# Kernel optimization log

Hardware: AMD Instinct MI355X
Metric: run time of the kernel (lower is better)

## Reference

```python
import jax, jax.numpy as jnp
import numpy as np

B, V, E = 1024, 50257, 128

def setup_inputs() -> dict:
    key = jax.random.key(0)
    k1, k2, k3 = jax.random.split(key, 3)
    # one-hot focus-word vectors [B, V]
    idx = jax.random.randint(k1, (B,), 0, V)
    xs = jax.nn.one_hot(idx, V, dtype=jnp.float32)
    EMBEDM = jax.random.normal(k2, (V, E), dtype=jnp.float32)
    metric = jax.random.normal(k3, (E, E), dtype=jnp.float32)
    return {"xs": xs, "EMBEDM": EMBEDM, "metric": metric}

def reference(xs, EMBEDM, metric):
    # xsembeds = xs @ EMBEDM  -> [B, E] (dense matmul that is mathematically a gather)
    xsembeds = jnp.matmul(xs, EMBEDM)
    # dots(vs, ws, metric) = (vs @ metric) @ ws.T -> [B, V]
    scores = jnp.matmul(jnp.matmul(xsembeds, metric), EMBEDM.T)
    return jax.nn.log_softmax(scores, axis=1)
```

## Files before the change

### kernel.cpp

```cpp
#include <hip/hip_runtime.h>
#include <math.h>

#define BB 1024
#define VV 50257
#define EE 128
#define RR 256
#define CC 1024
#define CH 64
#define NCH (CC / CH)
#define NCB ((VV + CC - 1) / CC)
#define CVTB 2048

typedef __bf16 bf16x8 __attribute__((ext_vector_type(8)));
typedef float f32x4 __attribute__((ext_vector_type(4)));
typedef f32x4 __attribute__((aligned(4))) f32x4u;

typedef __attribute__((address_space(3))) void as3_void;
typedef const __attribute__((address_space(1))) void as1_void;

static __device__ __forceinline__ unsigned short f2bf(float f) {
  unsigned int u = __float_as_uint(f);
  u += 0x7fffu + ((u >> 16) & 1u);
  return (unsigned short)(u >> 16);
}

__global__ __launch_bounds__(256) void k_prep(const float* __restrict__ xs,
                                              const float* __restrict__ em,
                                              const float* __restrict__ metric,
                                              unsigned short* __restrict__ ebf,
                                              unsigned short* __restrict__ ybf) {
  const int t = threadIdx.x;
  if (blockIdx.x < BB) {
    const int b = blockIdx.x;
    __shared__ int found;
    __shared__ int sidx;
    __shared__ float sval;
    __shared__ float x[EE];
    const float* row = xs + (size_t)b * VV;
    if (t == 0) {
      found = 0; sidx = 0; sval = 0.f;
      const float tail = row[VV - 1];
      if (tail != 0.f) { sidx = VV - 1; sval = tail; found = 1; }
    }
    __syncthreads();
    if (!found) {
      for (int base = 0; base < 12564; base += 1024) {
#pragma unroll
        for (int j = 0; j < 4; j++) {
          const int i = base + j * 256 + t;
          if (i < 12564) {
            f32x4u v = *(const f32x4u*)(row + i * 4);
            if (v[0] != 0.f || v[1] != 0.f || v[2] != 0.f || v[3] != 0.f) {
#pragma unroll
              for (int c = 0; c < 4; c++)
                if (v[c] != 0.f) { sidx = i * 4 + c; sval = v[c]; }
              found = 1;
            }
          }
        }
        __syncthreads();
        if (found) break;
      }
    }
    if (t < EE) x[t] = em[(size_t)sidx * EE + t] * sval;
    __syncthreads();
    if (t < EE) {
      float acc = 0.f;
#pragma unroll
      for (int k = 0; k < EE; k++) acc = fmaf(x[k], metric[k * EE + t], acc);
      ybf[b * EE + t] = f2bf(acc);
    }
  } else {
    const int total4 = VV * EE / 4;
    const int stride = CVTB * 256;
    for (int i = (blockIdx.x - BB) * 256 + t; i < total4; i += stride) {
      float4 v = ((const float4*)em)[i];
      ushort4 o;
      o.x = f2bf(v.x); o.y = f2bf(v.y); o.z = f2bf(v.z); o.w = f2bf(v.w);
      ((ushort4*)ebf)[i] = o;
    }
  }
}


static __device__ __forceinline__ void stageE(const unsigned short* __restrict__ ebf,
                                              char* ldsbuf, int colbase, int w, int lane) {
#pragma unroll
  for (int i = 0; i < 2; i++) {
    const int G = (i * 8 + w) * 64 + lane;
    const int c2 = G >> 4;
    const int gc = G & 15;
    int col = colbase + c2;
    col = col < VV ? col : VV - 1;
    const char* src = (const char*)(ebf + (size_t)col * EE) + ((gc ^ (c2 & 7)) * 16);
    __builtin_amdgcn_global_load_lds((as1_void*)src,
                                     (as3_void*)(ldsbuf + (i * 8 + w) * 1024), 16, 0, 0);
  }
}

template <bool PASS_B, bool TAIL>
static __device__ __forceinline__ void gemm_body(const unsigned short* __restrict__ ybf,
                                                 const unsigned short* __restrict__ ebf,
                                                 char* __restrict__ ldsE,
                                                 float* __restrict__ pm, float* __restrict__ ps,
                                                 const float* __restrict__ lse,
                                                 float* __restrict__ out) {
  const int cbx = blockIdx.x;
  const int rowbase = blockIdx.y * RR;
  const int w = threadIdx.x >> 6;
  const int l = threadIdx.x & 63;
  const int g = l >> 4;
  const int li = l & 15;
  const int rg = w >> 1;
  const int cg = w & 1;
  const int cb = cbx * CC;

  bf16x8 y[4][4];
#pragma unroll
  for (int rf = 0; rf < 4; rf++) {
    const bf16x8* yv = (const bf16x8*)(ybf + (size_t)(rowbase + rg * 64 + rf * 16 + li) * EE);
#pragma unroll
    for (int kk = 0; kk < 4; kk++) y[rf][kk] = yv[kk * 4 + g];
  }

  float Lr[4];
  float m[4], s[4];
  if (PASS_B) {
#pragma unroll
    for (int rf = 0; rf < 4; rf++) Lr[rf] = lse[rowbase + rg * 64 + rf * 16 + li];
  } else {
#pragma unroll
    for (int rf = 0; rf < 4; rf++) { m[rf] = -INFINITY; s[rf] = 0.f; }
  }

  stageE(ebf, ldsE, cb, w, l);
  __syncthreads();

#pragma unroll 2
  for (int k = 0; k < NCH; k++) {
    if (k + 1 < NCH) stageE(ebf, ldsE + ((k + 1) & 1) * 16384, cb + (k + 1) * CH, w, l);

    const char* cur = ldsE + (k & 1) * 16384;
    bf16x8 afr[2][4];
#pragma unroll
    for (int cf = 0; cf < 2; cf++) {
      const int c2 = cg * 32 + cf * 16 + li;
      const char* ebase = cur + c2 * 256;
#pragma unroll
      for (int kk = 0; kk < 4; kk++)
        afr[cf][kk] = *(const bf16x8*)(ebase + (((kk * 4 + g) ^ (li & 7)) * 16));
    }

    f32x4 acc[4][2];
#pragma unroll
    for (int rf = 0; rf < 4; rf++)
#pragma unroll
      for (int cf = 0; cf < 2; cf++) acc[rf][cf] = (f32x4){0.f, 0.f, 0.f, 0.f};
#pragma unroll
    for (int rf = 0; rf < 4; rf++)
#pragma unroll
      for (int cf = 0; cf < 2; cf++)
#pragma unroll
        for (int kk = 0; kk < 4; kk++)
          acc[rf][cf] = __builtin_amdgcn_mfma_f32_16x16x32_bf16(afr[cf][kk], y[rf][kk],
                                                                acc[rf][cf], 0, 0, 0);

    const int colk = cb + k * CH + cg * 32 + g * 4;

    if (!PASS_B) {
#pragma unroll
      for (int rf = 0; rf < 4; rf++) {
        float cm = -INFINITY;
#pragma unroll
        for (int cf = 0; cf < 2; cf++)
#pragma unroll
          for (int r = 0; r < 4; r++)
            if (!TAIL || colk + cf * 16 + r < VV) cm = fmaxf(cm, acc[rf][cf][r]);
        const float mn = fmaxf(m[rf], cm);
        if (!TAIL || mn > -INFINITY) {
          float as = s[rf] * __expf(m[rf] - mn);
#pragma unroll
          for (int cf = 0; cf < 2; cf++)
#pragma unroll
            for (int r = 0; r < 4; r++)
              if (!TAIL || colk + cf * 16 + r < VV) as += __expf(acc[rf][cf][r] - mn);
          s[rf] = as; m[rf] = mn;
        }
      }
    } else {
#pragma unroll
      for (int rf = 0; rf < 4; rf++) {
        float* orow = out + (size_t)(rowbase + rg * 64 + rf * 16 + li) * VV;
#pragma unroll
        for (int cf = 0; cf < 2; cf++) {
          const int c = colk + cf * 16;
          if (!TAIL || c + 3 < VV) {
            f32x4 v;
#pragma unroll
            for (int r = 0; r < 4; r++) v[r] = acc[rf][cf][r] - Lr[rf];
            *(f32x4u*)(orow + c) = v;
          } else {
#pragma unroll
            for (int r = 0; r < 4; r++)
              if (c + r < VV) orow[c + r] = acc[rf][cf][r] - Lr[rf];
          }
        }
      }
    }

    __syncthreads();
  }

  if (!PASS_B) {
#pragma unroll
    for (int off = 16; off <= 32; off <<= 1) {
#pragma unroll
      for (int rf = 0; rf < 4; rf++) {
        const float mo = __shfl_xor(m[rf], off);
        const float so = __shfl_xor(s[rf], off);
        const float mn = fmaxf(m[rf], mo);
        float sn;
        if (mn == -INFINITY) sn = 0.f;
        else sn = s[rf] * __expf(m[rf] - mn) + so * __expf(mo - mn);
        m[rf] = mn; s[rf] = sn;
      }
    }
    float* scm = (float*)ldsE;
    float* scs = scm + 512;
    __syncthreads();
    if (l < 16) {
#pragma unroll
      for (int rf = 0; rf < 4; rf++) {
        const int slot = ((rg * 2 + cg) * 4 + rf) * 16 + li;
        scm[slot] = m[rf]; scs[slot] = s[rf];
      }
    }
    __syncthreads();
    const int t = threadIdx.x;
    if (t < 256) {
      const int trg = t >> 6, trf = (t >> 4) & 3, tli = t & 15;
      const int s0 = ((trg * 2 + 0) * 4 + trf) * 16 + tli;
      const int s1 = ((trg * 2 + 1) * 4 + trf) * 16 + tli;
      const float m0 = scm[s0], m1 = scm[s1];
      const float mn = fmaxf(m0, m1);
      float sn;
      if (mn == -INFINITY) sn = 0.f;
      else sn = scs[s0] * __expf(m0 - mn) + scs[s1] * __expf(m1 - mn);
      const int grow = rowbase + trg * 64 + trf * 16 + tli;
      pm[(size_t)cbx * BB + grow] = mn;
      ps[(size_t)cbx * BB + grow] = sn;
    }
  }
}

__global__ __launch_bounds__(512) void k_gemm_a(const unsigned short* __restrict__ ybf,
                                                const unsigned short* __restrict__ ebf,
                                                float* __restrict__ pm,
                                                float* __restrict__ ps) {
  __shared__ char ldsE[2][16384];
  if (blockIdx.x < NCB - 1)
    gemm_body<false, false>(ybf, ebf, ldsE[0], pm, ps, nullptr, nullptr);
  else
    gemm_body<false, true>(ybf, ebf, ldsE[0], pm, ps, nullptr, nullptr);
}

__global__ __launch_bounds__(512) void k_gemm_b(const unsigned short* __restrict__ ybf,
                                                const unsigned short* __restrict__ ebf,
                                                const float* __restrict__ lse,
                                                float* __restrict__ out) {
  __shared__ char ldsE[2][16384];
  if (blockIdx.x < NCB - 1)
    gemm_body<true, false>(ybf, ebf, ldsE[0], nullptr, nullptr, lse, out);
  else
    gemm_body<true, true>(ybf, ebf, ldsE[0], nullptr, nullptr, lse, out);
}

__global__ void k_lse(const float* __restrict__ pm, const float* __restrict__ ps,
                      float* __restrict__ lse) {
  const int row = blockIdx.x;
  const int t = threadIdx.x;
  float m = (t < NCB) ? pm[(size_t)t * BB + row] : -INFINITY;
#pragma unroll
  for (int off = 32; off; off >>= 1) m = fmaxf(m, __shfl_xor(m, off));
  float s = (t < NCB) ? ps[(size_t)t * BB + row] * __expf(pm[(size_t)t * BB + row] - m) : 0.f;
#pragma unroll
  for (int off = 32; off; off >>= 1) s += __shfl_xor(s, off);
  if (t == 0) lse[row] = m + logf(s);
}

extern "C" void kernel_launch(void* const* d_in, const int* in_sizes, int n_in,
                              void* d_out, int out_size, void* d_ws, size_t ws_size,
                              hipStream_t stream) {
  const float* xs = (const float*)d_in[0];
  const float* em = (const float*)d_in[1];
  const float* metric = (const float*)d_in[2];
  float* out = (float*)d_out;

  char* w = (char*)d_ws;
  float* lse = (float*)(w + 8192);
  unsigned short* ybf = (unsigned short*)(w + 12288);
  unsigned short* ebf = (unsigned short*)(w + 12288 + 262144);
  float* pm = (float*)(w + 12288 + 262144 + 12865792);
  float* ps = (float*)(w + 12288 + 262144 + 12865792 + (size_t)NCB * BB * 4);

  k_prep<<<BB + CVTB, 256, 0, stream>>>(xs, em, metric, ebf, ybf);
  k_gemm_a<<<dim3(NCB, BB / RR), 512, 0, stream>>>(ybf, ebf, pm, ps);
  k_lse<<<BB, 64, 0, stream>>>(pm, ps, lse);
  k_gemm_b<<<dim3(NCB, BB / RR), 512, 0, stream>>>(ybf, ebf, lse, out);
}
```

Baseline: 150.5 us.

## Repartition vocab into 64 overlapping column blocks with ownership masking

Splits the vocabulary into 64 column blocks of 896 columns, each owning 786 columns, instead of 50 blocks of 1024, so the grid divides more evenly across compute units. The last block is clamped to start at VV-CC and overlaps its neighbour, which removes the tail-specialised template path. Softmax statistics count only the owned columns, while pass B writes the whole window, so overlapping columns get the same value written twice. In exchange the overlap adds redundant GEMM work and duplicate output stores, and the per-element ownership checks add comparisons in pass A.

```diff
diff --git a/kernel.cpp b/kernel.cpp
--- a/kernel.cpp
+++ b/kernel.cpp
@@ -5,10 +5,12 @@
 #define VV 50257
 #define EE 128
 #define RR 256
-#define CC 1024
+#define CC 896
 #define CH 64
 #define NCH (CC / CH)
-#define NCB ((VV + CC - 1) / CC)
+#define NCB 64
+#define OWN 786
+#define CBMAX (VV - CC)
 #define CVTB 2048
 
 typedef __bf16 bf16x8 __attribute__((ext_vector_type(8)));
@@ -98,7 +100,7 @@
   }
 }
 
-template <bool PASS_B, bool TAIL>
+template <bool PASS_B>
 static __device__ __forceinline__ void gemm_body(const unsigned short* __restrict__ ybf,
                                                  const unsigned short* __restrict__ ebf,
                                                  char* __restrict__ ldsE,
@@ -113,7 +115,10 @@
   const int li = l & 15;
   const int rg = w >> 1;
   const int cg = w & 1;
-  const int cb = cbx * CC;
+  const int own_lo = cbx * OWN;
+  const int own_hi = own_lo + OWN < VV ? own_lo + OWN : VV;
+  int cb = own_lo;
+  if (cb > CBMAX) cb = CBMAX;
 
   bf16x8 y[4][4];
 #pragma unroll
@@ -174,16 +179,20 @@
 #pragma unroll
         for (int cf = 0; cf < 2; cf++)
 #pragma unroll
-          for (int r = 0; r < 4; r++)
-            if (!TAIL || colk + cf * 16 + r < VV) cm = fmaxf(cm, acc[rf][cf][r]);
+          for (int r = 0; r < 4; r++) {
+            const int cv = colk + cf * 16 + r;
+            if (cv >= own_lo && cv < own_hi) cm = fmaxf(cm, acc[rf][cf][r]);
+          }
         const float mn = fmaxf(m[rf], cm);
-        if (!TAIL || mn > -INFINITY) {
+        if (mn > -INFINITY) {
           float as = s[rf] * __expf(m[rf] - mn);
 #pragma unroll
           for (int cf = 0; cf < 2; cf++)
 #pragma unroll
-            for (int r = 0; r < 4; r++)
-              if (!TAIL || colk + cf * 16 + r < VV) as += __expf(acc[rf][cf][r] - mn);
+            for (int r = 0; r < 4; r++) {
+              const int cv = colk + cf * 16 + r;
+              if (cv >= own_lo && cv < own_hi) as += __expf(acc[rf][cf][r] - mn);
+            }
           s[rf] = as; m[rf] = mn;
         }
       }
@@ -194,16 +203,10 @@
 #pragma unroll
         for (int cf = 0; cf < 2; cf++) {
           const int c = colk + cf * 16;
-          if (!TAIL || c + 3 < VV) {
-            f32x4 v;
-#pragma unroll
-            for (int r = 0; r < 4; r++) v[r] = acc[rf][cf][r] - Lr[rf];
-            *(f32x4u*)(orow + c) = v;
-          } else {
-#pragma unroll
-            for (int r = 0; r < 4; r++)
-              if (c + r < VV) orow[c + r] = acc[rf][cf][r] - Lr[rf];
-          }
+          f32x4 v;
+#pragma unroll
+          for (int r = 0; r < 4; r++) v[r] = acc[rf][cf][r] - Lr[rf];
+          *(f32x4u*)(orow + c) = v;
         }
       }
     }
@@ -258,10 +261,7 @@
                                                 float* __restrict__ pm,
                                                 float* __restrict__ ps) {
   __shared__ char ldsE[2][16384];
-  if (blockIdx.x < NCB - 1)
-    gemm_body<false, false>(ybf, ebf, ldsE[0], pm, ps, nullptr, nullptr);
-  else
-    gemm_body<false, true>(ybf, ebf, ldsE[0], pm, ps, nullptr, nullptr);
+  gemm_body<false>(ybf, ebf, ldsE[0], pm, ps, nullptr, nullptr);
 }
 
 __global__ __launch_bounds__(512) void k_gemm_b(const unsigned short* __restrict__ ybf,
@@ -269,20 +269,17 @@
                                                 const float* __restrict__ lse,
                                                 float* __restrict__ out) {
   __shared__ char ldsE[2][16384];
-  if (blockIdx.x < NCB - 1)
-    gemm_body<true, false>(ybf, ebf, ldsE[0], nullptr, nullptr, lse, out);
-  else
-    gemm_body<true, true>(ybf, ebf, ldsE[0], nullptr, nullptr, lse, out);
+  gemm_body<true>(ybf, ebf, ldsE[0], nullptr, nullptr, lse, out);
 }
 
 __global__ void k_lse(const float* __restrict__ pm, const float* __restrict__ ps,
                       float* __restrict__ lse) {
   const int row = blockIdx.x;
   const int t = threadIdx.x;
-  float m = (t < NCB) ? pm[(size_t)t * BB + row] : -INFINITY;
+  float m = pm[(size_t)t * BB + row];
 #pragma unroll
   for (int off = 32; off; off >>= 1) m = fmaxf(m, __shfl_xor(m, off));
-  float s = (t < NCB) ? ps[(size_t)t * BB + row] * __expf(pm[(size_t)t * BB + row] - m) : 0.f;
+  float s = ps[(size_t)t * BB + row] * __expf(pm[(size_t)t * BB + row] - m);
 #pragma unroll
   for (int off = 32; off; off >>= 1) s += __shfl_xor(s, off);
   if (t == 0) lse[row] = m + logf(s);
```

Result: no change. 149.8 us, median of 2 (-0.5%).
